# Kernel optimization log

Measured on AMD Instinct MI355X. Metric: run time of the kernel, lower is better.

The kernel has to match this reference:

```python
import jax, jax.numpy as jnp
import numpy as np

B, S, D, H = 32, 512, 512, 8  # note: source requires S == D due to swapped shape tuple in multi_head_attention
DK = D // H  # 64
FF = 200     # hard-coded FFN width in source
LN_EPS = 1e-5


def setup_inputs() -> dict:
    key = jax.random.key(0)
    ks = jax.random.split(key, 20)
    s = 0.02
    return {
        "x": jax.random.normal(ks[0], (B, S, D), dtype=jnp.float32),
        # per-head projections, stacked: torch Linear weight shape is [out, in] = [DK, D]
        "Wq": jax.random.normal(ks[1], (H, DK, D), dtype=jnp.float32) * s,
        "bq": jax.random.normal(ks[2], (H, DK), dtype=jnp.float32) * s,
        "Wk": jax.random.normal(ks[3], (H, DK, D), dtype=jnp.float32) * s,
        "bk": jax.random.normal(ks[4], (H, DK), dtype=jnp.float32) * s,
        "Wv": jax.random.normal(ks[5], (H, DK, D), dtype=jnp.float32) * s,
        "bv": jax.random.normal(ks[6], (H, DK), dtype=jnp.float32) * s,
        "Wo": jax.random.normal(ks[7], (D, D), dtype=jnp.float32) * s,
        "bo": jax.random.normal(ks[8], (D,), dtype=jnp.float32) * s,
        "W1": jax.random.normal(ks[9], (FF, D), dtype=jnp.float32) * s,
        "b1": jax.random.normal(ks[10], (FF,), dtype=jnp.float32) * s,
        "W2": jax.random.normal(ks[11], (FF, FF), dtype=jnp.float32) * s,
        "b2": jax.random.normal(ks[12], (FF,), dtype=jnp.float32) * s,
        "W3": jax.random.normal(ks[13], (D, FF), dtype=jnp.float32) * s,
        "b3": jax.random.normal(ks[14], (D,), dtype=jnp.float32) * s,
        # single SHARED LayerNorm over last two dims (S, D)
        "gamma": jnp.ones((S, D), dtype=jnp.float32),
        "beta": jnp.zeros((S, D), dtype=jnp.float32),
    }


def _layernorm2d(y, gamma, beta):
    # torch LayerNorm(normalized_shape=(S, D)): normalize over last two axes, biased variance
    m = jnp.mean(y, axis=(-2, -1), keepdims=True)
    v = jnp.mean(jnp.square(y - m), axis=(-2, -1), keepdims=True)
    return (y - m) * jax.lax.rsqrt(v + LN_EPS) * gamma + beta


def reference(x, Wq, bq, Wk, bk, Wv, bv, Wo, bo, W1, b1, W2, b2, W3, b3, gamma, beta):
    # --- multi-head attention (vectorized over the original per-head Python loop) ---
    q = jnp.einsum('bsd,hkd->bhsk', x, Wq) + bq[None, :, None, :]
    k = jnp.einsum('bsd,hkd->bhsk', x, Wk) + bk[None, :, None, :]
    v = jnp.einsum('bsd,hkd->bhsk', x, Wv) + bv[None, :, None, :]
    scores = jnp.einsum('bhsk,bhtk->bhst', q, k) / jnp.sqrt(jnp.float32(DK))
    attn = jax.nn.softmax(scores, axis=-1)
    heads = jnp.einsum('bhst,bhtk->bhsk', attn, v)          # [B,H,S,DK]
    concat = heads.transpose(0, 2, 1, 3).reshape(B, S, D)    # concat heads along feature dim
    y = jnp.einsum('bsd,ed->bse', concat, Wo) + bo + x       # output proj + residual
    # --- post-attention LayerNorm (shared params) ---
    y = _layernorm2d(y, gamma, beta)
    # --- feed-forward: D -> 200 -> 200 -> D, residual, LayerNorm (same shared LN) ---
    f = jax.nn.relu(jnp.einsum('bsd,fd->bsf', y, W1) + b1)
    f = jax.nn.relu(jnp.einsum('bsf,gf->bsg', f, W2) + b2)
    f = jnp.einsum('bsf,df->bsd', f, W3) + b3
    y = _layernorm2d(f + y, gamma, beta)
    # --- final LayerNorm (same shared LN again) ---
    return _layernorm2d(y, gamma, beta)
```

## Files before the change

kernel.cpp:

```cpp
#include <hip/hip_runtime.h>
#include <hip/hip_bf16.h>
#include <stdint.h>

#define B_  32
#define S_  512
#define D_  512
#define H_  8
#define DK_ 64
#define FF_ 200
#define FFP 256
#define M_  (B_*S_)
#define MSD ((size_t)B_*S_*D_)
#define NQKV 1536

typedef __hip_bfloat16 bf16;
typedef __attribute__((ext_vector_type(8))) short short8;
typedef __attribute__((ext_vector_type(4))) float f32x4;
typedef __attribute__((ext_vector_type(4))) unsigned short us4;

__device__ inline float b2f(bf16 v) { return __bfloat162float(v); }
__device__ inline bf16  f2b(float v){ return __float2bfloat16(v); }
__device__ inline unsigned short f2bu(float v) {
  union { bf16 h; unsigned short u; } cv; cv.h = __float2bfloat16(v); return cv.u;
}
__device__ inline float bu2f(unsigned short u) {
  union { unsigned short u; bf16 h; } cv; cv.u = u; return b2f(cv.h);
}
__device__ __forceinline__ void async16(const bf16* g, bf16* l) {
  __builtin_amdgcn_global_load_lds((const __attribute__((address_space(1))) void*)g,
                                   (__attribute__((address_space(3))) void*)l, 16, 0, 0);
}

__global__ void detect_kernel(const unsigned short* __restrict__ xu, int* __restrict__ flag,
                              float* __restrict__ stats) {
  __shared__ int mx[256];
  const int tid = threadIdx.x;
  if (tid < 192) stats[tid] = 0.f;
  int m = 0;
  for (int i = tid * 2; i < 8192; i += 512) {
    int e = (xu[i] >> 7) & 0xFF;
    m = m > e ? m : e;
  }
  mx[tid] = m;
  __syncthreads();
  for (int st = 128; st; st >>= 1) {
    if (tid < st) mx[tid] = mx[tid] > mx[tid + st] ? mx[tid] : mx[tid + st];
    __syncthreads();
  }
  if (tid == 0) *flag = (mx[0] >= 0xC0) ? 1 : 0;
}

__global__ __launch_bounds__(256) void cvt_x8(const void* __restrict__ in, bf16* __restrict__ out,
                                              const int* __restrict__ flag) {
  const bool f32in = (*flag != 0);
  size_t i = ((size_t)blockIdx.x * 256 + threadIdx.x) * 8;
  const size_t stride = (size_t)gridDim.x * 256 * 8;
  for (; i < MSD; i += stride) {
    if (f32in) {
      const float4 a = ((const float4*)in)[i/4];
      const float4 b = ((const float4*)in)[i/4 + 1];
      uint4 o; unsigned short* po = (unsigned short*)&o;
      po[0]=f2bu(a.x); po[1]=f2bu(a.y); po[2]=f2bu(a.z); po[3]=f2bu(a.w);
      po[4]=f2bu(b.x); po[5]=f2bu(b.y); po[6]=f2bu(b.z); po[7]=f2bu(b.w);
      *(uint4*)((unsigned short*)out + i) = o;
    } else {
      *(uint4*)((unsigned short*)out + i) = *(const uint4*)((const unsigned short*)in + i);
    }
  }
}

struct Seg { const void* src; void* dst; int srcRows, srcK, dstK, total; };
struct Segs { Seg s[16]; unsigned int isbf; };

__global__ __launch_bounds__(256) void cvt_all(Segs sg, const int* __restrict__ flag) {
  const bool f32in = (*flag != 0);
  const int seg = blockIdx.x & 15;
  const Seg sd = sg.s[seg];
  const int stride = (gridDim.x >> 4) * 256;
  const bool nopad = (sd.srcK == sd.dstK);
  for (int i = (blockIdx.x >> 4) * 256 + threadIdx.x; i < sd.total; i += stride) {
    int sidx; bool valid;
    if (nopad) { sidx = i; valid = (i < sd.srcRows * sd.srcK); }
    else {
      int r = i / sd.dstK, c = i - r * sd.dstK;
      valid = (r < sd.srcRows) && (c < sd.srcK);
      sidx = r * sd.srcK + c;
    }
    float v = 0.f;
    if (valid) v = f32in ? ((const float*)sd.src)[sidx] : b2f(((const bf16*)sd.src)[sidx]);
    if (sg.isbf & (1u << seg)) ((unsigned short*)sd.dst)[i] = f2bu(v);
    else                       ((float*)sd.dst)[i] = v;
  }
}

template<int MODE, int STATS, typename OUT>
__global__ __launch_bounds__(256) void gemm_mfma(
    const bf16* __restrict__ A, const bf16* __restrict__ W, const float* __restrict__ bias,
    const bf16* __restrict__ R, OUT* __restrict__ C, int M, int N, int K,
    float* __restrict__ stats)
{
  __shared__ bf16 As[128 * 32];
  __shared__ bf16 Bs[128 * 32];
  const int tid  = threadIdx.x;
  const int bm   = blockIdx.x * 128;
  const int bn   = blockIdx.y * 128;
  const int w    = tid >> 6;
  const int lane = tid & 63;
  const int qd   = lane >> 4;
  const int ln   = lane & 15;
  const int wr   = (w >> 1) * 64;
  const int wc   = (w & 1) * 64;

  const int r0 = lane >> 2;
  const int ch = (lane & 3) * 8;
  const bf16* Ag0 = A + (size_t)(bm + w*16 + r0) * K + ch;
  const bf16* Ag1 = Ag0 + (size_t)64 * K;
  const bf16* Bg0 = W + (size_t)(bn + w*16 + r0) * K + ch;
  const bf16* Bg1 = Bg0 + (size_t)64 * K;
  bf16* Al0 = As + w*512 + lane*8;
  bf16* Al1 = Al0 + 2048;
  bf16* Bl0 = Bs + w*512 + lane*8;
  bf16* Bl1 = Bl0 + 2048;

  f32x4 acc[4][4] = {};

  for (int k0 = 0; k0 < K; k0 += 32) {
    async16(Ag0 + k0, Al0);
    async16(Ag1 + k0, Al1);
    async16(Bg0 + k0, Bl0);
    async16(Bg1 + k0, Bl1);
    __syncthreads();

    short8 af[4], bfr[4];
#pragma unroll
    for (int i = 0; i < 4; i++) af[i]  = *(const short8*)(As + (wr + i*16 + ln)*32 + qd*8);
#pragma unroll
    for (int j = 0; j < 4; j++) bfr[j] = *(const short8*)(Bs + (wc + j*16 + ln)*32 + qd*8);
#pragma unroll
    for (int i = 0; i < 4; i++)
#pragma unroll
      for (int j = 0; j < 4; j++)
        acc[i][j] = __builtin_amdgcn_mfma_f32_16x16x32_bf16(af[i], bfr[j], acc[i][j], 0, 0, 0);
    __syncthreads();
  }

  float s_acc = 0.f, ss_acc = 0.f;
#pragma unroll
  for (int i = 0; i < 4; i++) {
#pragma unroll
    for (int j = 0; j < 4; j++) {
      int n = bn + wc + j*16 + ln;
      float bval = bias[n];
#pragma unroll
      for (int rg = 0; rg < 4; rg++) {
        int m = bm + wr + i*16 + qd*4 + rg;
        float val = acc[i][j][rg] + bval;
        if (MODE == 1) val = fmaxf(val, 0.f);
        if (MODE == 2) val += b2f(R[(size_t)m * N + n]);
        if (STATS) { s_acc += val; ss_acc += val * val; }
        if (sizeof(OUT) == 4) ((float*)C)[(size_t)m * N + n] = val;
        else                  ((bf16*)C)[(size_t)m * N + n]  = f2b(val);
      }
    }
  }

  if (STATS) {
    float* red = (float*)As;
    red[tid] = s_acc; red[256 + tid] = ss_acc;
    __syncthreads();
    for (int st = 128; st; st >>= 1) {
      if (tid < st) { red[tid] += red[tid + st]; red[256 + tid] += red[256 + tid + st]; }
      __syncthreads();
    }
    if (tid == 0) {
      int b = bm >> 9;
      atomicAdd(&stats[b*2],     red[0]);
      atomicAdd(&stats[b*2 + 1], red[256]);
    }
  }
}

__global__ __launch_bounds__(1024, 4) void attn_lds(const bf16* __restrict__ qkv,
                                                    bf16* __restrict__ cat)
{
  __shared__ bf16 Ks[2 * 512 * 32];
  __shared__ bf16 Vs[64 * 520];
  __shared__ bf16 pbuf[16][16][40];

  const int tid  = threadIdx.x;
  const int w    = tid >> 6;
  const int lane = tid & 63;
  const int qd   = lane >> 4;
  const int ln   = lane & 15;
  const int bh   = blockIdx.x;
  const int b    = bh >> 3, h = bh & 7;
  const bf16* base = qkv + (size_t)b * 512 * NQKV + h * 64;

  for (int c = tid; c < 4096; c += 1024) {
    int part = c & 3, key = (c >> 2) & 511, ks = c >> 11;
    async16(base + (size_t)key * NQKV + 512 + ks*32 + part*8, Ks + c*8);
  }
  for (int c = tid; c < 4096; c += 1024) {
    int dkg = c & 7, key = c >> 3;
    uint4 vv = *(const uint4*)(base + (size_t)key * NQKV + 1024 + dkg*8);
    const unsigned short* pv = (const unsigned short*)&vv;
#pragma unroll
    for (int j = 0; j < 8; j++)
      *(unsigned short*)&Vs[(dkg*8 + j)*520 + key] = pv[j];
  }
  short8 bq[2][2];
#pragma unroll
  for (int qt = 0; qt < 2; qt++)
#pragma unroll
    for (int ks = 0; ks < 2; ks++)
      bq[qt][ks] = *(const short8*)(base + (size_t)(w*32 + qt*16 + ln) * NQKV + ks*32 + qd*8);

  __syncthreads();

  bf16 (*pb)[40] = pbuf[w];
  f32x4 o[2][4] = {};
  float l[2] = {0.f, 0.f};

  for (int st = 0; st < 16; st++) {
    short8 ak[2][2];
#pragma unroll
    for (int kt = 0; kt < 2; kt++)
#pragma unroll
      for (int ks = 0; ks < 2; ks++)
        ak[kt][ks] = *(const short8*)(Ks + ks*16384 + (st*32 + kt*16 + ln)*32 + qd*8);
    f32x4 s[2][2] = {};
#pragma unroll
    for (int kt = 0; kt < 2; kt++)
#pragma unroll
      for (int qt = 0; qt < 2; qt++) {
        s[kt][qt] = __builtin_amdgcn_mfma_f32_16x16x32_bf16(ak[kt][0], bq[qt][0], s[kt][qt], 0, 0, 0);
        s[kt][qt] = __builtin_amdgcn_mfma_f32_16x16x32_bf16(ak[kt][1], bq[qt][1], s[kt][qt], 0, 0, 0);
      }
    float e[2][2][4];
#pragma unroll
    for (int kt = 0; kt < 2; kt++)
#pragma unroll
      for (int qt = 0; qt < 2; qt++)
#pragma unroll
        for (int rg = 0; rg < 4; rg++) {
          float ev = __expf(s[kt][qt][rg] * 0.125f);
          e[kt][qt][rg] = ev;
          l[qt] += ev;
        }
#pragma unroll
    for (int qt = 0; qt < 2; qt++) {
#pragma unroll
      for (int kt = 0; kt < 2; kt++) {
        uint2 pk;
        pk.x = (unsigned)f2bu(e[kt][qt][0]) | ((unsigned)f2bu(e[kt][qt][1]) << 16);
        pk.y = (unsigned)f2bu(e[kt][qt][2]) | ((unsigned)f2bu(e[kt][qt][3]) << 16);
        *(uint2*)&pb[ln][kt*16 + qd*4] = pk;
      }
      short8 ap = *(const short8*)&pb[ln][qd*8];
#pragma unroll
      for (int nt = 0; nt < 4; nt++) {
        short8 bv = *(const short8*)(Vs + (nt*16 + ln)*520 + st*32 + qd*8);
        o[qt][nt] = __builtin_amdgcn_mfma_f32_16x16x32_bf16(ap, bv, o[qt][nt], 0, 0, 0);
      }
    }
  }

#pragma unroll
  for (int qt = 0; qt < 2; qt++) {
    l[qt] += __shfl_xor(l[qt], 16);
    l[qt] += __shfl_xor(l[qt], 32);
  }
  float inv0 = 1.f / l[0], inv1 = 1.f / l[1];

  const size_t crow0 = (size_t)(b*S_ + w*32) * D_ + h*DK_;
#pragma unroll
  for (int qt = 0; qt < 2; qt++) {
#pragma unroll
    for (int rg = 0; rg < 4; rg++) {
      float ivv = __shfl(qt ? inv1 : inv0, qd*4 + rg);
      int r = qt*16 + qd*4 + rg;
      bf16* cp = cat + crow0 + (size_t)r * D_ + ln;
#pragma unroll
      for (int nt = 0; nt < 4; nt++) cp[nt*16] = f2b(o[qt][nt][rg] * ivv);
    }
  }
}

__global__ __launch_bounds__(256) void ln_b16_b16(const bf16* __restrict__ in,
    const float* __restrict__ stats, const float* __restrict__ gamma,
    const float* __restrict__ beta, bf16* __restrict__ out)
{
  const int b = blockIdx.x >> 4;
  const float invN = 1.f / (float)(S_*D_);
  const float m    = stats[b*2] * invN;
  const float var  = stats[b*2+1] * invN - m*m;
  const float rstd = rsqrtf(var + 1e-5f);
  size_t v = (size_t)b * 65536 + (blockIdx.x & 15) * 4096 + threadIdx.x;
#pragma unroll 4
  for (int it = 0; it < 16; it++, v += 256) {
    us4 xi = *(const us4*)((const unsigned short*)in + v*4);
    size_t e = (v * 4) & (S_*D_ - 1);
    float4 g = *(const float4*)(gamma + e);
    float4 bt= *(const float4*)(beta + e);
    us4 o;
    o[0] = f2bu((bu2f(xi[0]) - m) * rstd * g.x + bt.x);
    o[1] = f2bu((bu2f(xi[1]) - m) * rstd * g.y + bt.y);
    o[2] = f2bu((bu2f(xi[2]) - m) * rstd * g.z + bt.z);
    o[3] = f2bu((bu2f(xi[3]) - m) * rstd * g.w + bt.w);
    *(us4*)((unsigned short*)out + v*4) = o;
  }
}

__global__ __launch_bounds__(256) void ln_b16_b16_stats(const bf16* __restrict__ in,
    const float* __restrict__ stats, const float* __restrict__ gamma,
    const float* __restrict__ beta, bf16* __restrict__ out, float* __restrict__ stats3)
{
  __shared__ float red[512];
  const int b = blockIdx.x >> 4;
  const float invN = 1.f / (float)(S_*D_);
  const float m    = stats[b*2] * invN;
  const float var  = stats[b*2+1] * invN - m*m;
  const float rstd = rsqrtf(var + 1e-5f);
  size_t v = (size_t)b * 65536 + (blockIdx.x & 15) * 4096 + threadIdx.x;
  float s_acc = 0.f, ss_acc = 0.f;
#pragma unroll 4
  for (int it = 0; it < 16; it++, v += 256) {
    us4 xi = *(const us4*)((const unsigned short*)in + v*4);
    size_t e = (v * 4) & (S_*D_ - 1);
    float4 g = *(const float4*)(gamma + e);
    float4 bt= *(const float4*)(beta + e);
    float o0 = (bu2f(xi[0]) - m) * rstd * g.x + bt.x;
    float o1 = (bu2f(xi[1]) - m) * rstd * g.y + bt.y;
    float o2 = (bu2f(xi[2]) - m) * rstd * g.z + bt.z;
    float o3 = (bu2f(xi[3]) - m) * rstd * g.w + bt.w;
    us4 o;
    o[0] = f2bu(o0); o[1] = f2bu(o1); o[2] = f2bu(o2); o[3] = f2bu(o3);
    s_acc  += o0 + o1 + o2 + o3;
    ss_acc += o0*o0 + o1*o1 + o2*o2 + o3*o3;
    *(us4*)((unsigned short*)out + v*4) = o;
  }
  const int tid = threadIdx.x;
  red[tid] = s_acc; red[256 + tid] = ss_acc;
  __syncthreads();
  for (int st = 128; st; st >>= 1) {
    if (tid < st) { red[tid] += red[tid + st]; red[256 + tid] += red[256 + tid + st]; }
    __syncthreads();
  }
  if (tid == 0) {
    atomicAdd(&stats3[b*2],     red[0]);
    atomicAdd(&stats3[b*2 + 1], red[256]);
  }
}

__global__ __launch_bounds__(256) void ln_apply_out(const bf16* __restrict__ in,
    const float* __restrict__ stats, const float* __restrict__ gamma,
    const float* __restrict__ beta, void* __restrict__ out, const int* __restrict__ flag)
{
  const bool f32 = (*flag != 0);
  const int b = blockIdx.x >> 4;
  const float invN = 1.f / (float)(S_*D_);
  const float m    = stats[b*2] * invN;
  const float var  = stats[b*2+1] * invN - m*m;
  const float rstd = rsqrtf(var + 1e-5f);
  size_t v = (size_t)b * 65536 + (blockIdx.x & 15) * 4096 + threadIdx.x;
#pragma unroll 4
  for (int it = 0; it < 16; it++, v += 256) {
    us4 xi = *(const us4*)((const unsigned short*)in + v*4);
    size_t e = (v * 4) & (S_*D_ - 1);
    float4 g = *(const float4*)(gamma + e);
    float4 bt= *(const float4*)(beta + e);
    float4 o;
    o.x = (bu2f(xi[0]) - m) * rstd * g.x + bt.x;
    o.y = (bu2f(xi[1]) - m) * rstd * g.y + bt.y;
    o.z = (bu2f(xi[2]) - m) * rstd * g.z + bt.z;
    o.w = (bu2f(xi[3]) - m) * rstd * g.w + bt.w;
    if (f32) ((float4*)out)[v] = o;
    else {
      us4 ob;
      ob[0] = f2bu(o.x); ob[1] = f2bu(o.y); ob[2] = f2bu(o.z); ob[3] = f2bu(o.w);
      *(us4*)((unsigned short*)out + v*4) = ob;
    }
  }
}

extern "C" void kernel_launch(void* const* d_in, const int* in_sizes, int n_in,
                              void* d_out, int out_size, void* d_ws, size_t ws_size,
                              hipStream_t stream)
{
  char* p = (char*)d_ws;
  auto alloc_b = [&](size_t elems) { void* r = p; p += elems * 2; return (bf16*)r; };
  auto alloc_f = [&](size_t elems) {
    p = (char*)(((uintptr_t)p + 15) & ~(uintptr_t)15); void* r = p; p += elems * 4; return (float*)r;
  };

  bf16* xb   = alloc_b(MSD);
  bf16* qkv  = alloc_b(3 * MSD);
  bf16* catb = alloc_b(MSD);
  bf16* wqkv = alloc_b(3 * 512 * 512);
  bf16* wo   = alloc_b(512 * 512);
  bf16* w1p  = alloc_b((size_t)FFP * 512);
  bf16* w2p  = alloc_b((size_t)FFP * FFP);
  bf16* w3p  = alloc_b((size_t)512 * FFP);
  float* bqkv= alloc_f(3 * 512);
  float* bo  = alloc_f(512);
  float* b1p = alloc_f(FFP);
  float* b2p = alloc_f(FFP);
  float* b3  = alloc_f(512);
  float* gm  = alloc_f((size_t)S_ * D_);
  float* bt  = alloc_f((size_t)S_ * D_);
  float* stats = alloc_f(192);
  int*   flag  = (int*)alloc_f(16);
  if ((size_t)(p - (char*)d_ws) > ws_size) return;

  bf16* y1b = qkv;
  bf16* f1  = qkv + MSD;
  bf16* f2  = qkv + MSD + (size_t)M_ * FFP;
  bf16* yA  = qkv + 2 * MSD;
  bf16* yB  = catb;
  bf16* y2b = yA;
  float* st1 = stats, *st2 = stats + 64, *st3 = stats + 128;

  detect_kernel<<<1, 256, 0, stream>>>((const unsigned short*)d_in[0], flag, stats);
  cvt_x8<<<2048, 256, 0, stream>>>(d_in[0], xb, flag);

  Segs sg;
  sg.s[0]  = { d_in[1],  wqkv,               512, 512, 512, 512*512 };
  sg.s[1]  = { d_in[3],  wqkv + 512*512,     512, 512, 512, 512*512 };
  sg.s[2]  = { d_in[5],  wqkv + 2*512*512,   512, 512, 512, 512*512 };
  sg.s[3]  = { d_in[7],  wo,                 512, 512, 512, 512*512 };
  sg.s[4]  = { d_in[9],  w1p,                FF_, 512, 512, FFP*512 };
  sg.s[5]  = { d_in[11], w2p,                FF_, FF_, FFP, FFP*FFP };
  sg.s[6]  = { d_in[13], w3p,                512, FF_, FFP, 512*FFP };
  sg.s[7]  = { d_in[2],  bqkv,               1, 512, 512, 512 };
  sg.s[8]  = { d_in[4],  bqkv + 512,         1, 512, 512, 512 };
  sg.s[9]  = { d_in[6],  bqkv + 1024,        1, 512, 512, 512 };
  sg.s[10] = { d_in[8],  bo,                 1, 512, 512, 512 };
  sg.s[11] = { d_in[10], b1p,                1, FF_, FFP, FFP };
  sg.s[12] = { d_in[12], b2p,                1, FF_, FFP, FFP };
  sg.s[13] = { d_in[14], b3,                 1, 512, 512, 512 };
  sg.s[14] = { d_in[15], gm,                 1, S_*D_, S_*D_, S_*D_ };
  sg.s[15] = { d_in[16], bt,                 1, S_*D_, S_*D_, S_*D_ };
  sg.isbf = 0x007F;
  cvt_all<<<1024, 256, 0, stream>>>(sg, flag);

  dim3 blk(256);

  gemm_mfma<0, 0, bf16><<<dim3(M_/128, NQKV/128), blk, 0, stream>>>(
      xb, wqkv, bqkv, nullptr, qkv, M_, NQKV, 512, nullptr);

  attn_lds<<<B_*H_, 1024, 0, stream>>>(qkv, catb);

  gemm_mfma<2, 1, bf16><<<dim3(M_/128, 4), blk, 0, stream>>>(
      catb, wo, bo, xb, yA, M_, 512, 512, st1);

  ln_b16_b16<<<512, blk, 0, stream>>>(yA, st1, gm, bt, y1b);

  gemm_mfma<1, 0, bf16><<<dim3(M_/128, 2), blk, 0, stream>>>(
      y1b, w1p, b1p, nullptr, f1, M_, FFP, 512, nullptr);
  gemm_mfma<1, 0, bf16><<<dim3(M_/128, 2), blk, 0, stream>>>(
      f1, w2p, b2p, nullptr, f2, M_, FFP, FFP, nullptr);
  gemm_mfma<2, 1, bf16><<<dim3(M_/128, 4), blk, 0, stream>>>(
      f2, w3p, b3, y1b, yB, M_, 512, FFP, st2);

  ln_b16_b16_stats<<<512, blk, 0, stream>>>(yB, st2, gm, bt, y2b, st3);
  ln_apply_out<<<512, blk, 0, stream>>>(y2b, st3, gm, bt, d_out, flag);
}
```

Measured before the change: 300.6 us.

## Double GEMM K-step to 64 and stage epilogue through LDS for vector stores

The shared MFMA GEMM now loads 64-wide K slices per iteration, which halves the number of barrier pairs per tile. The epilogue writes accumulators to a padded LDS tile and then does coalesced 16-byte reads of bias and residual and 16-byte bf16 stores, replacing the scattered 2-byte stores. This uses more LDS (32KB) and adds barriers in the epilogue, which could reduce occupancy. The float-output template path is removed.

```diff
diff --git a/kernel.cpp b/kernel.cpp
--- a/kernel.cpp
+++ b/kernel.cpp
@@ -93,14 +93,18 @@
   }
 }
 
-template<int MODE, int STATS, typename OUT>
+template<int MODE, int STATS>
 __global__ __launch_bounds__(256) void gemm_mfma(
     const bf16* __restrict__ A, const bf16* __restrict__ W, const float* __restrict__ bias,
-    const bf16* __restrict__ R, OUT* __restrict__ C, int M, int N, int K,
+    const bf16* __restrict__ R, bf16* __restrict__ C, int M, int N, int K,
     float* __restrict__ stats)
 {
-  __shared__ bf16 As[128 * 32];
-  __shared__ bf16 Bs[128 * 32];
+  __shared__ __align__(16) char smem[32768];
+  bf16*  As  = (bf16*)smem;
+  bf16*  Bs  = (bf16*)smem + 8192;
+  float* Lf  = (float*)smem;
+  float* red = (float*)(smem + 20480);
+
   const int tid  = threadIdx.x;
   const int bm   = blockIdx.x * 128;
   const int bn   = blockIdx.y * 128;
@@ -111,61 +115,93 @@
   const int wr   = (w >> 1) * 64;
   const int wc   = (w & 1) * 64;
 
-  const int r0 = lane >> 2;
-  const int ch = (lane & 3) * 8;
-  const bf16* Ag0 = A + (size_t)(bm + w*16 + r0) * K + ch;
-  const bf16* Ag1 = Ag0 + (size_t)64 * K;
-  const bf16* Bg0 = W + (size_t)(bn + w*16 + r0) * K + ch;
-  const bf16* Bg1 = Bg0 + (size_t)64 * K;
-  bf16* Al0 = As + w*512 + lane*8;
-  bf16* Al1 = Al0 + 2048;
-  bf16* Bl0 = Bs + w*512 + lane*8;
-  bf16* Bl1 = Bl0 + 2048;
+  const bf16* srcA[4]; const bf16* srcB[4];
+  bf16* dstA[4]; bf16* dstB[4];
+#pragma unroll
+  for (int i2 = 0; i2 < 4; i2++) {
+    const int g   = w*4 + i2;
+    const int row = (g & 7)*16 + (lane >> 2);
+    const int col = (g >> 3)*32 + (lane & 3)*8;
+    srcA[i2] = A + (size_t)(bm + row) * K + col;
+    srcB[i2] = W + (size_t)(bn + row) * K + col;
+    dstA[i2] = As + g*512 + lane*8;
+    dstB[i2] = Bs + g*512 + lane*8;
+  }
 
   f32x4 acc[4][4] = {};
 
-  for (int k0 = 0; k0 < K; k0 += 32) {
-    async16(Ag0 + k0, Al0);
-    async16(Ag1 + k0, Al1);
-    async16(Bg0 + k0, Bl0);
-    async16(Bg1 + k0, Bl1);
-    __syncthreads();
-
-    short8 af[4], bfr[4];
-#pragma unroll
-    for (int i = 0; i < 4; i++) af[i]  = *(const short8*)(As + (wr + i*16 + ln)*32 + qd*8);
-#pragma unroll
-    for (int j = 0; j < 4; j++) bfr[j] = *(const short8*)(Bs + (wc + j*16 + ln)*32 + qd*8);
-#pragma unroll
-    for (int i = 0; i < 4; i++)
-#pragma unroll
-      for (int j = 0; j < 4; j++)
-        acc[i][j] = __builtin_amdgcn_mfma_f32_16x16x32_bf16(af[i], bfr[j], acc[i][j], 0, 0, 0);
+  for (int k0 = 0; k0 < K; k0 += 64) {
+#pragma unroll
+    for (int i2 = 0; i2 < 4; i2++) {
+      async16(srcA[i2] + k0, dstA[i2]);
+      async16(srcB[i2] + k0, dstB[i2]);
+    }
+    __syncthreads();
+#pragma unroll
+    for (int kk = 0; kk < 2; kk++) {
+      short8 af[4], bfr[4];
+#pragma unroll
+      for (int i = 0; i < 4; i++) af[i]  = *(const short8*)(As + kk*4096 + (wr + i*16 + ln)*32 + qd*8);
+#pragma unroll
+      for (int j = 0; j < 4; j++) bfr[j] = *(const short8*)(Bs + kk*4096 + (wc + j*16 + ln)*32 + qd*8);
+#pragma unroll
+      for (int i = 0; i < 4; i++)
+#pragma unroll
+        for (int j = 0; j < 4; j++)
+          acc[i][j] = __builtin_amdgcn_mfma_f32_16x16x32_bf16(af[i], bfr[j], acc[i][j], 0, 0, 0);
+    }
     __syncthreads();
   }
 
   float s_acc = 0.f, ss_acc = 0.f;
+  const int lrbase = (w >> 1)*16 + qd*4;
 #pragma unroll
   for (int i = 0; i < 4; i++) {
 #pragma unroll
     for (int j = 0; j < 4; j++) {
-      int n = bn + wc + j*16 + ln;
-      float bval = bias[n];
-#pragma unroll
-      for (int rg = 0; rg < 4; rg++) {
-        int m = bm + wr + i*16 + qd*4 + rg;
-        float val = acc[i][j][rg] + bval;
-        if (MODE == 1) val = fmaxf(val, 0.f);
-        if (MODE == 2) val += b2f(R[(size_t)m * N + n]);
-        if (STATS) { s_acc += val; ss_acc += val * val; }
-        if (sizeof(OUT) == 4) ((float*)C)[(size_t)m * N + n] = val;
-        else                  ((bf16*)C)[(size_t)m * N + n]  = f2b(val);
+      const int col = wc + j*16 + ln;
+#pragma unroll
+      for (int rg = 0; rg < 4; rg++)
+        Lf[(lrbase + rg)*132 + col] = acc[i][j][rg];
+    }
+    __syncthreads();
+#pragma unroll
+    for (int pz = 0; pz < 2; pz++) {
+      const int q   = tid + pz*256;
+      const int r   = q >> 4;
+      const int nof = (q & 15)*8;
+      const int m   = bm + (r >> 4)*64 + i*16 + (r & 15);
+      const int n   = bn + nof;
+      f32x4 v0 = *(const f32x4*)(Lf + r*132 + nof);
+      f32x4 v1 = *(const f32x4*)(Lf + r*132 + nof + 4);
+      f32x4 b0 = *(const f32x4*)(bias + n);
+      f32x4 b1 = *(const f32x4*)(bias + n + 4);
+      float vals[8];
+#pragma unroll
+      for (int e = 0; e < 4; e++) { vals[e] = v0[e] + b0[e]; vals[4+e] = v1[e] + b1[e]; }
+      if (MODE == 1) {
+#pragma unroll
+        for (int e = 0; e < 8; e++) vals[e] = fmaxf(vals[e], 0.f);
       }
-    }
+      if (MODE == 2) {
+        const uint4 rv = *(const uint4*)((const unsigned short*)R + (size_t)m * N + n);
+        const unsigned short* rp = (const unsigned short*)&rv;
+#pragma unroll
+        for (int e = 0; e < 8; e++) vals[e] += bu2f(rp[e]);
+      }
+      if (STATS) {
+#pragma unroll
+        for (int e = 0; e < 8; e++) { s_acc += vals[e]; ss_acc += vals[e]*vals[e]; }
+      }
+      uint4 o; unsigned short* op = (unsigned short*)&o;
+#pragma unroll
+      for (int e = 0; e < 8; e++) op[e] = f2bu(vals[e]);
+      *(uint4*)((unsigned short*)C + (size_t)m * N + n) = o;
+    }
+    __syncthreads();
   }
 
   if (STATS) {
-    float* red = (float*)As;
     red[tid] = s_acc; red[256 + tid] = ss_acc;
     __syncthreads();
     for (int st = 128; st; st >>= 1) {
@@ -173,7 +209,7 @@
       __syncthreads();
     }
     if (tid == 0) {
-      int b = bm >> 9;
+      const int b = bm >> 9;
       atomicAdd(&stats[b*2],     red[0]);
       atomicAdd(&stats[b*2 + 1], red[256]);
     }
@@ -445,21 +481,21 @@
 
   dim3 blk(256);
 
-  gemm_mfma<0, 0, bf16><<<dim3(M_/128, NQKV/128), blk, 0, stream>>>(
+  gemm_mfma<0, 0><<<dim3(M_/128, NQKV/128), blk, 0, stream>>>(
       xb, wqkv, bqkv, nullptr, qkv, M_, NQKV, 512, nullptr);
 
   attn_lds<<<B_*H_, 1024, 0, stream>>>(qkv, catb);
 
-  gemm_mfma<2, 1, bf16><<<dim3(M_/128, 4), blk, 0, stream>>>(
+  gemm_mfma<2, 1><<<dim3(M_/128, 4), blk, 0, stream>>>(
       catb, wo, bo, xb, yA, M_, 512, 512, st1);
 
   ln_b16_b16<<<512, blk, 0, stream>>>(yA, st1, gm, bt, y1b);
 
-  gemm_mfma<1, 0, bf16><<<dim3(M_/128, 2), blk, 0, stream>>>(
+  gemm_mfma<1, 0><<<dim3(M_/128, 2), blk, 0, stream>>>(
       y1b, w1p, b1p, nullptr, f1, M_, FFP, 512, nullptr);
-  gemm_mfma<1, 0, bf16><<<dim3(M_/128, 2), blk, 0, stream>>>(
+  gemm_mfma<1, 0><<<dim3(M_/128, 2), blk, 0, stream>>>(
       f1, w2p, b2p, nullptr, f2, M_, FFP, FFP, nullptr);
-  gemm_mfma<2, 1, bf16><<<dim3(M_/128, 4), blk, 0, stream>>>(
+  gemm_mfma<2, 1><<<dim3(M_/128, 4), blk, 0, stream>>>(
       f2, w3p, b3, y1b, yB, M_, 512, FFP, st2);
 
   ln_b16_b16_stats<<<512, blk, 0, stream>>>(yB, st2, gm, bt, y2b, st3);
```

Result: faster. 294.5 us (-2.0%).
